# Optimization experiments

Measured on AMD Instinct MI355X. Metric: run time of the kernel, lower is better.

Reference implementation:

```python
import jax, jax.numpy as jnp
import numpy as np

D = 1024; H = 16; HD = 64; DEPTH = 8; INTERVAL = 4; CTX = 9; NUM_REG = 4
SOFTCAP = 50.0; EPS = 1e-6; ROPE_BASE = 10000.0; IN_DIM = 768; ADIM = 8; FREQ = 256; DH = 4096
B = 1; T = 16; LTOK = 256; S = LTOK + 2 + NUM_REG  # 262 tokens per frame


def setup_inputs() -> dict:
    key = jax.random.key(0)
    ks = jax.random.split(key, 24)
    s = 0.02
    n = jax.random.normal
    inp = {
        'noisy_latents': n(ks[0], (B, T, LTOK, IN_DIM), jnp.float32),
        'signal_levels': jax.random.uniform(ks[1], (B, T), jnp.float32),
        'actions': n(ks[2], (B, T, ADIM), jnp.float32),
        'input_proj_w': n(ks[3], (D, IN_DIM)) * s,
        'noise_w1': n(ks[4], (D, FREQ)) * s,
        'noise_b1': jnp.zeros((D,)),
        'noise_w2': n(ks[5], (D, D)) * s,
        'noise_b2': jnp.zeros((D,)),
        'base_action_embed': n(ks[6], (D,)) * s,
        'action_proj_w': n(ks[7], (D, ADIM)) * (s * 0.1),
        'action_proj_b': jnp.zeros((D,)),
        'register_tokens': n(ks[8], (NUM_REG, D)) * s,
        'ln1_w': jnp.ones((DEPTH, D)),
        's_wqkv': n(ks[9], (DEPTH, 3 * D, D)) * s,
        's_wo': n(ks[10], (DEPTH, D, D)) * s,
        's_qg': jnp.ones((DEPTH, HD)),
        's_kg': jnp.ones((DEPTH, HD)),
        'lnt_w': jnp.ones((DEPTH, D)),
        't_wqkv': n(ks[11], (DEPTH, 3 * D, D)) * s,
        't_wo': n(ks[12], (DEPTH, D, D)) * s,
        't_qg': jnp.ones((DEPTH, HD)),
        't_kg': jnp.ones((DEPTH, HD)),
        'ln2_w': jnp.ones((DEPTH, D)),
        'mlp_w12': n(ks[13], (DEPTH, 2 * DH, D)) * s,
        'mlp_w3': n(ks[14], (DEPTH, D, DH)) * s,
        'final_norm_w': jnp.ones((D,)),
        'out_w': n(ks[15], (IN_DIM, D)) * s,
        'out_b': jnp.zeros((IN_DIM,)),
    }
    return inp


def rms(x, w, eps=EPS):
    return x * jax.lax.rsqrt(jnp.mean(x * x, axis=-1, keepdims=True) + eps) * w


def rope_cache(seq_len):
    inv = ROPE_BASE ** (-jnp.arange(0, HD, 2, dtype=jnp.float32) / HD)  # [HD/2]
    f = jnp.arange(seq_len, dtype=jnp.float32)[:, None] * inv  # [S, HD/2]
    return jnp.cos(f), jnp.sin(f)


def apply_rope(x, cos, sin):
    # x: [..., S, HD]; cos/sin: [S, HD/2]
    x1, x2 = jnp.split(x, 2, axis=-1)
    return jnp.concatenate([x1 * cos - x2 * sin, x1 * sin + x2 * cos], axis=-1)


def attention(xn, wqkv, wo, qg, kg, cos, sin, mask):
    # xn: [B, G, S, D]; mask broadcastable to [..., S, S]
    lead = xn.shape[:-1]
    qkv = jnp.einsum('bgsd,ed->bgse', xn, wqkv)
    q, k, v = jnp.split(qkv, 3, axis=-1)
    def heads(z):
        return z.reshape(lead + (H, HD)).swapaxes(-2, -3)  # [B, G, H, S, HD]
    q, k, v = heads(q), heads(k), heads(v)
    q = rms(q, qg); k = rms(k, kg)  # qk-norm per head
    q = apply_rope(q, cos, sin); k = apply_rope(k, cos, sin)
    logits = jnp.einsum('bghqd,bghkd->bghqk', q, k) / np.sqrt(HD).astype(np.float32)
    logits = SOFTCAP * jnp.tanh(logits / SOFTCAP)  # attn logit softcapping
    logits = jnp.where(mask, logits, -1e30)
    p = jax.nn.softmax(logits, axis=-1)
    o = jnp.einsum('bghqk,bghkd->bghqd', p, v)
    o = o.swapaxes(-2, -3).reshape(lead + (H * HD,))
    return jnp.einsum('bgsd,ed->bgse', o, wo)


def timestep_embedding(t, dim=FREQ, max_period=10000.0):
    half = dim // 2
    freqs = jnp.exp(-np.log(max_period) * jnp.arange(half, dtype=jnp.float32) / half)
    args = t[:, None] * freqs
    return jnp.concatenate([jnp.cos(args), jnp.sin(args)], axis=-1)


def reference(noisy_latents, signal_levels, actions, input_proj_w, noise_w1, noise_b1,
              noise_w2, noise_b2, base_action_embed, action_proj_w, action_proj_b,
              register_tokens, ln1_w, s_wqkv, s_wo, s_qg, s_kg, lnt_w, t_wqkv, t_wo,
              t_qg, t_kg, ln2_w, mlp_w12, mlp_w3, final_norm_w, out_w, out_b):
    b, t, ltok, _ = noisy_latents.shape
    noisy_tokens = jnp.einsum('btld,ed->btle', noisy_latents, input_proj_w)  # [B,T,L,D]
    # timestep embedder (sinusoidal + MLP)
    emb = timestep_embedding(signal_levels.reshape(-1))
    sig = jax.nn.silu(emb @ noise_w1.T + noise_b1) @ noise_w2.T + noise_b2
    sig = sig.reshape(b, t, 1, D)
    act = base_action_embed + actions @ action_proj_w.T + action_proj_b  # [B,T,D]
    act = act[:, :, None, :]
    reg = jnp.broadcast_to(register_tokens, (b, t, NUM_REG, D))
    x = jnp.concatenate([sig, act, reg, noisy_tokens], axis=2)  # [B,T,S,D]
    s = x.shape[2]
    # spatial mask: full attention except frozen token (row 0) attends only to itself
    sm = jnp.ones((s, s), bool)
    sm = sm.at[0].set(False).at[0, 0].set(True)
    # temporal mask: causal with context window CTX
    ti = jnp.arange(t)
    tm = (ti[None, :] <= ti[:, None]) & (ti[None, :] >= ti[:, None] - CTX)
    s_cos, s_sin = rope_cache(s)
    t_cos, t_sin = rope_cache(t)
    for l in range(DEPTH):
        h = rms(x, ln1_w[l])
        x = x + attention(h, s_wqkv[l], s_wo[l], s_qg[l], s_kg[l], s_cos, s_sin, sm)
        if l % INTERVAL == 0:
            xt = x.swapaxes(1, 2)  # [B,S,T,D]
            h = rms(xt, lnt_w[l])
            xt = xt + attention(h, t_wqkv[l], t_wo[l], t_qg[l], t_kg[l], t_cos, t_sin, tm)
            x = xt.swapaxes(1, 2)
        h = rms(x, ln2_w[l])
        g = jnp.einsum('btsd,ed->btse', h, mlp_w12[l])
        g1, g2 = jnp.split(g, 2, axis=-1)
        x = x + jnp.einsum('btse,de->btsd', jax.nn.silu(g1) * g2, mlp_w3[l])
    latents = rms(x[..., NUM_REG + 2:, :], final_norm_w)
    return latents @ out_w.T + out_b  # [B,T,L,IN_DIM]
```

## Files before the change

### kernel.cpp

```cpp
#include <hip/hip_runtime.h>
#include <hip/hip_bf16.h>
#include <math.h>

#define T_ 16
#define S_ 262
#define D_ 1024
#define H_ 16
#define HD_ 64
#define DH_ 4096
#define NTOK (T_*S_)
#define LTOK_ 256
#define INDIM_ 768

typedef __attribute__((ext_vector_type(4))) float f32x4;
typedef __attribute__((ext_vector_type(8))) short s16x8;
typedef __attribute__((ext_vector_type(4))) short s16x4;

__device__ __forceinline__ short f2bf(float f) {
  union { float f; unsigned u; } v; v.f = f;
  unsigned r = v.u + 0x7fffu + ((v.u >> 16) & 1u);
  return (short)(r >> 16);
}
__device__ __forceinline__ float bf2f(short h) {
  union { unsigned u; float f; } v; v.u = ((unsigned)(unsigned short)h) << 16;
  return v.f;
}
__device__ __forceinline__ float softcap(float x) {
  float z = __expf(x * (2.0f / 50.0f));
  return 50.0f * (z - 1.0f) / (z + 1.0f);
}
__device__ __forceinline__ void gload16(const void* g, void* l) {
  __builtin_amdgcn_global_load_lds((const __attribute__((address_space(1))) void*)g,
                                   (__attribute__((address_space(3))) void*)l, 16, 0, 0);
}

template<int RESID, int BIAS, int OUT, int WB, int PERM, int PREP, int ROWMAP>
__global__ __launch_bounds__(256)
void gemm2(const short* __restrict__ A, const void* __restrict__ Wv,
           const float* __restrict__ bias, void* __restrict__ Cv,
           int M, int N, int K, int Ksub,
           const float* __restrict__ qg, const float* __restrict__ kg,
           const float* __restrict__ ctab, const float* __restrict__ stab)
{
  __shared__ __align__(16) short As[128*64];
  __shared__ __align__(16) short Bs[128*64];
  const int tid = threadIdx.x;
  const int m0 = blockIdx.y * 128, n0 = blockIdx.x * 128;
  const int lane = tid & 63, wid = tid >> 6;
  const int wr = (wid >> 1) * 64, wc = (wid & 1) * 64;
  const int lr = lane & 15, lk = (lane >> 4) * 8;
  const short* Wb = (const short*)Wv;
  const float* Wf = (const float*)Wv;

  const f32x4 fzero = {0.f, 0.f, 0.f, 0.f};
  f32x4 acc[4][4];
  #pragma unroll
  for (int i = 0; i < 4; ++i)
    #pragma unroll
    for (int j = 0; j < 4; ++j) acc[i][j] = fzero;

  const int kbeg = blockIdx.z * Ksub;
  for (int k0 = kbeg; k0 < kbeg + Ksub; k0 += 64) {
    #pragma unroll
    for (int i = 0; i < 4; ++i) {
      int row = wid*32 + i*8 + (lane >> 3);
      int gm = m0 + row; if (gm >= M) gm = M - 1;
      int gc = (((lane & 7) ^ (row & 7)) << 3);
      gload16(A + (size_t)gm*K + k0 + gc, &As[(wid*32 + i*8)*64]);
    }
    if (WB) {
      #pragma unroll
      for (int i = 0; i < 4; ++i) {
        int row = wid*32 + i*8 + (lane >> 3);
        int gc = (((lane & 7) ^ (row & 7)) << 3);
        gload16(Wb + (size_t)(n0 + row)*K + k0 + gc, &Bs[(wid*32 + i*8)*64]);
      }
    } else {
      #pragma unroll
      for (int i = 0; i < 4; ++i) {
        int slot = tid + 256*i;
        int row = slot >> 3, c8 = (slot & 7) << 3;
        int gr = n0 + row;
        if (PERM) { int c = gr >> 5, q = gr & 31; gr = (q < 16) ? c*16 + q : DH_ + c*16 + (q - 16); }
        const float* wp = Wf + (size_t)gr*K + k0 + c8;
        float4 w0 = *(const float4*)wp, w1 = *(const float4*)(wp + 4);
        s16x8 b;
        b[0]=f2bf(w0.x); b[1]=f2bf(w0.y); b[2]=f2bf(w0.z); b[3]=f2bf(w0.w);
        b[4]=f2bf(w1.x); b[5]=f2bf(w1.y); b[6]=f2bf(w1.z); b[7]=f2bf(w1.w);
        *(s16x8*)&Bs[row*64 + (c8 ^ ((row & 7) << 3))] = b;
      }
    }
    __syncthreads();
    #pragma unroll
    for (int kh = 0; kh < 2; ++kh) {
      const int col0 = kh*32 + lk;
      s16x8 af[4], bfr[4];
      #pragma unroll
      for (int mi = 0; mi < 4; ++mi) {
        int row = wr + mi*16 + lr;
        af[mi] = *(const s16x8*)&As[row*64 + (col0 ^ ((row & 7) << 3))];
      }
      #pragma unroll
      for (int ni = 0; ni < 4; ++ni) {
        int row = wc + ni*16 + lr;
        bfr[ni] = *(const s16x8*)&Bs[row*64 + (col0 ^ ((row & 7) << 3))];
      }
      #pragma unroll
      for (int mi = 0; mi < 4; ++mi)
        #pragma unroll
        for (int ni = 0; ni < 4; ++ni)
          acc[mi][ni] = __builtin_amdgcn_mfma_f32_16x16x32_bf16(af[mi], bfr[ni], acc[mi][ni], 0, 0, 0);
    }
    __syncthreads();
  }
  const int gg = (lane >> 4) * 4;
  if (OUT == 2) {
    #pragma unroll
    for (int mi = 0; mi < 4; ++mi)
      #pragma unroll
      for (int np = 0; np < 2; ++np) {
        const int ni = np*2;
        const int ocol = ((n0 + wc + ni*16) >> 5) * 16 + lr;
        #pragma unroll
        for (int r = 0; r < 4; ++r) {
          int row = m0 + wr + mi*16 + gg + r;
          if (row < M) {
            float g = acc[mi][ni][r], v = acc[mi][ni+1][r];
            float sl = g / (1.f + __expf(-g));
            ((short*)Cv)[(size_t)row * (N >> 1) + ocol] = f2bf(sl * v);
          }
        }
      }
  } else if (PREP) {
    const int colsec = n0 + wc;
    const bool isv = (colsec >= 2048);
    const float* gp = (colsec < 1024) ? qg : kg;
    float gv[4];
    if (!isv) {
      #pragma unroll
      for (int ni = 0; ni < 4; ++ni) gv[ni] = gp[ni*16 + lr];
    }
    #pragma unroll
    for (int mi = 0; mi < 4; ++mi) {
      #pragma unroll
      for (int r = 0; r < 4; ++r) {
        int row = m0 + wr + mi*16 + gg + r;
        int rowc = row < M ? row : M - 1;
        float vv[4];
        #pragma unroll
        for (int ni = 0; ni < 4; ++ni) vv[ni] = acc[mi][ni][r];
        if (!isv) {
          float ss = vv[0]*vv[0] + vv[1]*vv[1] + vv[2]*vv[2] + vv[3]*vv[3];
          ss += __shfl_xor(ss, 1);
          ss += __shfl_xor(ss, 2);
          ss += __shfl_xor(ss, 4);
          ss += __shfl_xor(ss, 8);
          float sc = rsqrtf(ss * (1.f/64.f) + 1e-6f);
          int pos = (PREP == 1) ? (rowc % S_) : (rowc / S_);
          float c0 = ctab[pos*32 + lr],      s0 = stab[pos*32 + lr];
          float c1 = ctab[pos*32 + 16 + lr], s1 = stab[pos*32 + 16 + lr];
          float a0 = vv[0]*sc*gv[0], a1 = vv[1]*sc*gv[1];
          float a2 = vv[2]*sc*gv[2], a3 = vv[3]*sc*gv[3];
          vv[0] = a0*c0 - a2*s0;
          vv[1] = a1*c1 - a3*s1;
          vv[2] = a0*s0 + a2*c0;
          vv[3] = a1*s1 + a3*c1;
        }
        if (row < M) {
          #pragma unroll
          for (int ni = 0; ni < 4; ++ni)
            ((short*)Cv)[(size_t)row * N + n0 + wc + ni*16 + lr] = f2bf(vv[ni]);
        }
      }
    }
  } else {
    #pragma unroll
    for (int mi = 0; mi < 4; ++mi)
      #pragma unroll
      for (int ni = 0; ni < 4; ++ni) {
        int col = n0 + wc + ni*16 + lr;
        #pragma unroll
        for (int r = 0; r < 4; ++r) {
          int row = m0 + wr + mi*16 + gg + r;
          if (row < M) {
            float v = acc[mi][ni][r];
            if (BIAS) v += bias[col];
            size_t orow = ROWMAP ? (size_t)((row >> 8) * S_ + 6 + (row & 255)) : (size_t)row;
            size_t idx = orow * N + col;
            if (RESID == 1)       ((float*)Cv)[idx] += v;
            else if (RESID == 2)  unsafeAtomicAdd(&((float*)Cv)[idx], v);
            else if (OUT == 1)    ((short*)Cv)[idx]  = f2bf(v);
            else                  ((float*)Cv)[idx]  = v;
          }
        }
      }
  }
}

template<int FINAL>
__global__ __launch_bounds__(256)
void rmsnorm_k(const float* __restrict__ x, const float* __restrict__ w, short* __restrict__ h)
{
  const int lane = threadIdx.x & 63;
  const int row = blockIdx.x*4 + (threadIdx.x >> 6);
  const int xrow = FINAL ? ((row >> 8) * S_ + 6 + (row & 255)) : row;
  const float* xp = x + (size_t)xrow*D_;
  float4 v[4];
  #pragma unroll
  for (int j = 0; j < 4; ++j) v[j] = *(const float4*)(xp + j*256 + lane*4);
  float ss = 0.f;
  #pragma unroll
  for (int j = 0; j < 4; ++j) ss += v[j].x*v[j].x + v[j].y*v[j].y + v[j].z*v[j].z + v[j].w*v[j].w;
  #pragma unroll
  for (int m = 1; m < 64; m <<= 1) ss += __shfl_xor(ss, m);
  const float sc = rsqrtf(ss * (1.f/1024.f) + 1e-6f);
  #pragma unroll
  for (int j = 0; j < 4; ++j) {
    float4 wv = *(const float4*)(w + j*256 + lane*4);
    s16x4 hv;
    hv[0] = f2bf(v[j].x*sc*wv.x); hv[1] = f2bf(v[j].y*sc*wv.y);
    hv[2] = f2bf(v[j].z*sc*wv.z); hv[3] = f2bf(v[j].w*sc*wv.w);
    *(s16x4*)(h + (size_t)row*D_ + j*256 + lane*4) = hv;
  }
}

__global__ void rope_tab_k(float* __restrict__ ct, float* __restrict__ st, int npos)
{
  int i = blockIdx.x*256 + threadIdx.x;
  if (i >= npos*32) return;
  int pos = i >> 5, fi = i & 31;
  float ang = (float)pos * expf((float)fi * (-9.210340371976184f/32.f));
  float s, c; sincosf(ang, &s, &c);
  ct[i] = c; st[i] = s;
}

__global__ __launch_bounds__(256)
void attn_spatial_k(const short* __restrict__ qkv, short* __restrict__ o)
{
  __shared__ __align__(16) short Vt[64][296];
  __shared__ __align__(16) short Pl[4][16][296];
  const int tid = threadIdx.x;
  const int b = blockIdx.x;
  const int t = b >> 4, h = b & 15;
// ... 105 lines not shown
  const int s = gw >> 4, h = gw & 15;
  const int tt = lane >> 2, dp = (lane & 3) * 16;
  const short* base = qkv + (size_t)(tt*S_ + s)*3072 + h*64 + dp;
  #pragma unroll
  for (int part = 0; part < 3; ++part) {
    const short* bp = base + part*1024;
    s16x8 v0 = *(const s16x8*)(bp);
    s16x8 v1 = *(const s16x8*)(bp + 8);
    float* dst = (part == 0) ? &Ql[wid][tt][dp] : (part == 1) ? &Kl[wid][tt][dp] : &Vl[wid][tt][dp];
    #pragma unroll
    for (int j = 0; j < 8; ++j) { dst[j] = bf2f(v0[j]); dst[8 + j] = bf2f(v1[j]); }
  }
  __syncthreads();
  const int qr = lane >> 2;
  float qv[64];
  #pragma unroll
  for (int j = 0; j < 64; ++j) qv[j] = Ql[wid][qr][j];
  float pvals[4];
  #pragma unroll
  for (int i = 0; i < 4; ++i) {
    int kt = (lane & 3) + i*4;
    float d = 0.f;
    #pragma unroll
    for (int j = 0; j < 64; ++j) d += qv[j] * Kl[wid][kt][j];
    d *= 0.125f;
    d = softcap(d);
    bool keep = (kt <= qr) && (kt + 9 >= qr);
    pvals[i] = keep ? d : -1e30f;
  }
  float mx = fmaxf(fmaxf(pvals[0], pvals[1]), fmaxf(pvals[2], pvals[3]));
  mx = fmaxf(mx, __shfl_xor(mx, 1));
  mx = fmaxf(mx, __shfl_xor(mx, 2));
  float sum = 0.f;
  #pragma unroll
  for (int i = 0; i < 4; ++i) { pvals[i] = __expf(pvals[i] - mx); sum += pvals[i]; }
  sum += __shfl_xor(sum, 1);
  sum += __shfl_xor(sum, 2);
  float is = 1.f / sum;
  #pragma unroll
  for (int i = 0; i < 4; ++i) Pl2[wid][qr][(lane & 3) + i*4] = pvals[i] * is;
  __syncthreads();
  float acc[16];
  #pragma unroll
  for (int j = 0; j < 16; ++j) acc[j] = 0.f;
  #pragma unroll
  for (int kt = 0; kt < 16; ++kt) {
    float pv = Pl2[wid][qr][kt];
    #pragma unroll
    for (int j = 0; j < 16; ++j) acc[j] += pv * Vl[wid][kt][dp + j];
  }
  short* op = o + (size_t)(qr*S_ + s)*D_ + h*64 + dp;
  #pragma unroll
  for (int j = 0; j < 16; ++j) op[j] = f2bf(acc[j]);
}

__global__ void cvt_f32_bf16_k(const float* __restrict__ in, short* __restrict__ out, int n4)
{
  int i = blockIdx.x*256 + threadIdx.x;
  if (i >= n4) return;
  float4 v = *(const float4*)(in + (size_t)i*4);
  s16x4 ov; ov[0]=f2bf(v.x); ov[1]=f2bf(v.y); ov[2]=f2bf(v.z); ov[3]=f2bf(v.w);
  *(s16x4*)(out + (size_t)i*4) = ov;
}

__global__ void cvt_w12_k(const float* __restrict__ in, short* __restrict__ out)
{
  int pb = blockIdx.x;
  int l = pb >> 13, pr = pb & 8191;
  int c = pr >> 5, q = pr & 31;
  int orig = (q < 16) ? c*16 + q : DH_ + c*16 + (q - 16);
  const float* ip = in + ((size_t)l*8192 + orig)*1024 + threadIdx.x*4;
  short* op = out + ((size_t)l*8192 + pr)*1024 + threadIdx.x*4;
  float4 v = *(const float4*)ip;
  s16x4 ov; ov[0]=f2bf(v.x); ov[1]=f2bf(v.y); ov[2]=f2bf(v.z); ov[3]=f2bf(v.w);
  *(s16x4*)op = ov;
}

__global__ void timestep_embed_k(const float* __restrict__ sig, float* __restrict__ emb)
{
  int tid = threadIdx.x;
  int n = tid >> 4;
  int j0 = (tid & 15) * 16;
  float tv = sig[n];
  for (int j = j0; j < j0 + 16; ++j) {
    int half = j & 127;
    float freq = expf(-9.210340371976184f * (float)half / 128.f);
    float a = tv * freq;
    emb[n*256 + j] = (j < 128) ? cosf(a) : sinf(a);
  }
}

__global__ void noise_mlp1_k(const float* __restrict__ emb, const float* __restrict__ w1,
                             const float* __restrict__ b1, float* __restrict__ hid)
{
  const int o = blockIdx.x*256 + threadIdx.x;
  const int n = o >> 10, e = o & 1023;
  const float4* er = (const float4*)(emb + n*256);
  const float4* wr = (const float4*)(w1 + (size_t)e*256);
  float s = b1[e];
  for (int k = 0; k < 64; ++k) { float4 a = er[k]; float4 b = wr[k]; s += a.x*b.x + a.y*b.y + a.z*b.z + a.w*b.w; }
  hid[o] = s / (1.f + __expf(-s));
}

__global__ void noise_mlp2_k(const float* __restrict__ hid, const float* __restrict__ w2,
                             const float* __restrict__ b2, float* __restrict__ sg)
{
// ... 43 lines not shown
  const float* nw1     = (const float*)d_in[4];
  const float* nb1     = (const float*)d_in[5];
  const float* nw2     = (const float*)d_in[6];
  const float* nb2     = (const float*)d_in[7];
  const float* base_ae = (const float*)d_in[8];
  const float* apw     = (const float*)d_in[9];
  const float* apb     = (const float*)d_in[10];
  const float* regtok  = (const float*)d_in[11];
  const float* ln1w    = (const float*)d_in[12];
  const float* s_wqkv  = (const float*)d_in[13];
  const float* s_wo    = (const float*)d_in[14];
  const float* s_qg    = (const float*)d_in[15];
  const float* s_kg    = (const float*)d_in[16];
  const float* lntw    = (const float*)d_in[17];
  const float* t_wqkv  = (const float*)d_in[18];
  const float* t_wo    = (const float*)d_in[19];
  const float* t_qg    = (const float*)d_in[20];
  const float* t_kg    = (const float*)d_in[21];
  const float* ln2w    = (const float*)d_in[22];
  const float* w12     = (const float*)d_in[23];
  const float* w3      = (const float*)d_in[24];
  const float* fnw     = (const float*)d_in[25];
  const float* outw    = (const float*)d_in[26];
  const float* outb    = (const float*)d_in[27];

  char* p = (char*)d_ws;
  auto take = [&](size_t n) { char* r = p; p += n; return r; };
  float* x   = (float*)take((size_t)NTOK*D_*4);
  short* hb  = (short*)take((size_t)NTOK*D_*2);
  short* qkv = (short*)take((size_t)NTOK*3072*2);
  short* ob  = (short*)take((size_t)NTOK*D_*2);
  short* mb  = qkv;
  short* nlb = (short*)take((size_t)4096*INDIM_*2);
  float* emb = (float*)take(16*256*4);
  float* hid = (float*)take(16*1024*4);
  float* sgb = (float*)take(16*1024*4);
  float* acr = (float*)take(16*1024*4);
  float* csS = (float*)take(S_*32*4);
  float* snS = (float*)take(S_*32*4);
  float* csT = (float*)take(16*32*4);
  float* snT = (float*)take(16*32*4);
  short* wqkv_s_bf = (short*)take((size_t)8*3*D_*D_*2);
  short* wo_s_bf   = (short*)take((size_t)8*D_*D_*2);
  short* wqkv_t_bf = (short*)take((size_t)2*3*D_*D_*2);
  short* wo_t_bf   = (short*)take((size_t)2*D_*D_*2);
  short* w12_bf    = (short*)take((size_t)8*2*DH_*D_*2);
  short* w3_bf     = (short*)take((size_t)8*D_*DH_*2);
  short* inp_bf    = (short*)take((size_t)D_*INDIM_*2);
  short* outw_bf   = (short*)take((size_t)INDIM_*D_*2);
  const size_t full_need = (size_t)(p - (char*)d_ws);
  const bool wb = ws_size >= full_need;

  if (wb) {
    cvt_f32_bf16_k<<<24576, 256, 0, stream>>>(s_wqkv, wqkv_s_bf, 8*3*D_*D_/4);
    cvt_f32_bf16_k<<<8192,  256, 0, stream>>>(s_wo,   wo_s_bf,   8*D_*D_/4);
    cvt_f32_bf16_k<<<3072,  256, 0, stream>>>(t_wqkv,                     wqkv_t_bf,                   3*D_*D_/4);
    cvt_f32_bf16_k<<<3072,  256, 0, stream>>>(t_wqkv + (size_t)4*3*D_*D_, wqkv_t_bf + (size_t)3*D_*D_, 3*D_*D_/4);
    cvt_f32_bf16_k<<<1024,  256, 0, stream>>>(t_wo,                       wo_t_bf,                     D_*D_/4);
    cvt_f32_bf16_k<<<1024,  256, 0, stream>>>(t_wo + (size_t)4*D_*D_,     wo_t_bf + (size_t)D_*D_,     D_*D_/4);
    cvt_w12_k<<<65536, 256, 0, stream>>>(w12, w12_bf);
    cvt_f32_bf16_k<<<32768, 256, 0, stream>>>(w3, w3_bf, 8*D_*DH_/4);
    cvt_f32_bf16_k<<<768,   256, 0, stream>>>(in_proj, inp_bf, D_*INDIM_/4);
    cvt_f32_bf16_k<<<768,   256, 0, stream>>>(outw, outw_bf, INDIM_*D_/4);
  }
  rope_tab_k<<<33, 256, 0, stream>>>(csS, snS, S_);
  rope_tab_k<<<2,  256, 0, stream>>>(csT, snT, 16);

  timestep_embed_k<<<1, 256, 0, stream>>>(sig_lv, emb);
  noise_mlp1_k<<<64, 256, 0, stream>>>(emb, nw1, nb1, hid);
  noise_mlp2_k<<<64, 256, 0, stream>>>(hid, nw2, nb2, sgb);
  act_embed_k<<<64, 256, 0, stream>>>(actions, base_ae, apw, apb, acr);
  cvt_f32_bf16_k<<<3072, 256, 0, stream>>>(noisy, nlb, 4096*INDIM_/4);
  if (wb) gemm2<0,0,0,1,0,0,1><<<dim3(8,32), 256, 0, stream>>>(nlb, inp_bf,  nullptr, x, 4096, D_, INDIM_, INDIM_, nullptr, nullptr, nullptr, nullptr);
  else    gemm2<0,0,0,0,0,0,1><<<dim3(8,32), 256, 0, stream>>>(nlb, in_proj, nullptr, x, 4096, D_, INDIM_, INDIM_, nullptr, nullptr, nullptr, nullptr);
  fill6_k<<<96, 256, 0, stream>>>(sgb, acr, regtok, x);

  for (int l = 0; l < 8; ++l) {
    rmsnorm_k<0><<<NTOK/4, 256, 0, stream>>>(x, ln1w + l*D_, hb);
    if (wb) gemm2<0,0,1,1,0,1,0><<<dim3(24,33), 256, 0, stream>>>(hb, wqkv_s_bf + (size_t)l*3*D_*D_, nullptr, qkv, NTOK, 3*D_, D_, D_, s_qg + l*HD_, s_kg + l*HD_, csS, snS);
    else    gemm2<0,0,1,0,0,1,0><<<dim3(24,33), 256, 0, stream>>>(hb, s_wqkv   + (size_t)l*3*D_*D_, nullptr, qkv, NTOK, 3*D_, D_, D_, s_qg + l*HD_, s_kg + l*HD_, csS, snS);
    attn_spatial_k<<<256, 256, 0, stream>>>(qkv, ob);
    if (wb) gemm2<1,0,0,1,0,0,0><<<dim3(8,33), 256, 0, stream>>>(ob, wo_s_bf + (size_t)l*D_*D_, nullptr, x, NTOK, D_, D_, D_, nullptr, nullptr, nullptr, nullptr);
    else    gemm2<1,0,0,0,0,0,0><<<dim3(8,33), 256, 0, stream>>>(ob, s_wo    + (size_t)l*D_*D_, nullptr, x, NTOK, D_, D_, D_, nullptr, nullptr, nullptr, nullptr);
    if (l % 4 == 0) {
      const int ls = l / 4;
      rmsnorm_k<0><<<NTOK/4, 256, 0, stream>>>(x, lntw + l*D_, hb);
      if (wb) gemm2<0,0,1,1,0,2,0><<<dim3(24,33), 256, 0, stream>>>(hb, wqkv_t_bf + (size_t)ls*3*D_*D_, nullptr, qkv, NTOK, 3*D_, D_, D_, t_qg + l*HD_, t_kg + l*HD_, csT, snT);
      else    gemm2<0,0,1,0,0,2,0><<<dim3(24,33), 256, 0, stream>>>(hb, t_wqkv    + (size_t)l*3*D_*D_,  nullptr, qkv, NTOK, 3*D_, D_, D_, t_qg + l*HD_, t_kg + l*HD_, csT, snT);
      attn_temporal_k<<<1048, 256, 0, stream>>>(qkv, ob);
      if (wb) gemm2<1,0,0,1,0,0,0><<<dim3(8,33), 256, 0, stream>>>(ob, wo_t_bf + (size_t)ls*D_*D_, nullptr, x, NTOK, D_, D_, D_, nullptr, nullptr, nullptr, nullptr);
      else    gemm2<1,0,0,0,0,0,0><<<dim3(8,33), 256, 0, stream>>>(ob, t_wo    + (size_t)l*D_*D_,  nullptr, x, NTOK, D_, D_, D_, nullptr, nullptr, nullptr, nullptr);
    }
    rmsnorm_k<0><<<NTOK/4, 256, 0, stream>>>(x, ln2w + l*D_, hb);
    if (wb) gemm2<0,0,2,1,0,0,0><<<dim3(64,33), 256, 0, stream>>>(hb, w12_bf + (size_t)l*2*DH_*D_, nullptr, mb, NTOK, 2*DH_, D_, D_, nullptr, nullptr, nullptr, nullptr);
    else    gemm2<0,0,2,0,1,0,0><<<dim3(64,33), 256, 0, stream>>>(hb, w12    + (size_t)l*2*DH_*D_, nullptr, mb, NTOK, 2*DH_, D_, D_, nullptr, nullptr, nullptr, nullptr);
    if (wb) gemm2<2,0,0,1,0,0,0><<<dim3(8,33,2), 256, 0, stream>>>(mb, w3_bf + (size_t)l*D_*DH_, nullptr, x, NTOK, D_, DH_, DH_/2, nullptr, nullptr, nullptr, nullptr);
    else    gemm2<2,0,0,0,0,0,0><<<dim3(8,33,2), 256, 0, stream>>>(mb, w3    + (size_t)l*D_*DH_, nullptr, x, NTOK, D_, DH_, DH_/2, nullptr, nullptr, nullptr, nullptr);
  }
  rmsnorm_k<1><<<1024, 256, 0, stream>>>(x, fnw, hb);
  if (wb) gemm2<0,1,0,1,0,0,0><<<dim3(6,32), 256, 0, stream>>>(hb, outw_bf, outb, (float*)d_out, 4096, INDIM_, D_, D_, nullptr, nullptr, nullptr, nullptr);
  else    gemm2<0,1,0,0,0,0,0><<<dim3(6,32), 256, 0, stream>>>(hb, outw,    outb, (float*)d_out, 4096, INDIM_, D_, D_, nullptr, nullptr, nullptr, nullptr);
}
```

Measured before the change: 3.386 ms.

## Add 64x64 GEMM tile variant for N=1024 GEMMs and drop split-K atomics

Adds a SMALL template mode giving 64x64 output tiles, and uses it for the narrow GEMMs (input projection, Wo projections, MLP down-projection, output head) so they launch more blocks. The down-projection no longer splits K with atomic adds and now accumulates over the full K=4096 in one block with a plain residual add. All weight conversions except w12 are batched into one multi-job conversion kernel. Smaller tiles lower data reuse per block and raise the number of loads per MFMA, in exchange for better occupancy and no atomic traffic.

```diff
diff --git a/kernel.cpp b/kernel.cpp
--- a/kernel.cpp
+++ b/kernel.cpp
@@ -34,50 +34,53 @@
                                    (__attribute__((address_space(3))) void*)l, 16, 0, 0);
 }
 
-template<int RESID, int BIAS, int OUT, int WB, int PERM, int PREP, int ROWMAP>
+template<int SMALL, int RESID, int BIAS, int OUT, int WB, int PERM, int PREP, int ROWMAP>
 __global__ __launch_bounds__(256)
 void gemm2(const short* __restrict__ A, const void* __restrict__ Wv,
            const float* __restrict__ bias, void* __restrict__ Cv,
-           int M, int N, int K, int Ksub,
+           int M, int N, int K,
            const float* __restrict__ qg, const float* __restrict__ kg,
            const float* __restrict__ ctab, const float* __restrict__ stab)
 {
-  __shared__ __align__(16) short As[128*64];
-  __shared__ __align__(16) short Bs[128*64];
+  constexpr int BM   = SMALL ? 64 : 128;
+  constexpr int MI   = SMALL ? 2 : 4;
+  constexpr int WR   = SMALL ? 32 : 64;
+  constexpr int NSTG = SMALL ? 2 : 4;
+  __shared__ __align__(16) short As[BM*64];
+  __shared__ __align__(16) short Bs[BM*64];
   const int tid = threadIdx.x;
-  const int m0 = blockIdx.y * 128, n0 = blockIdx.x * 128;
+  const int m0 = blockIdx.y * BM, n0 = blockIdx.x * BM;
   const int lane = tid & 63, wid = tid >> 6;
-  const int wr = (wid >> 1) * 64, wc = (wid & 1) * 64;
+  const int wr = (wid >> 1) * WR, wc = (wid & 1) * WR;
   const int lr = lane & 15, lk = (lane >> 4) * 8;
   const short* Wb = (const short*)Wv;
   const float* Wf = (const float*)Wv;
 
   const f32x4 fzero = {0.f, 0.f, 0.f, 0.f};
-  f32x4 acc[4][4];
-  #pragma unroll
-  for (int i = 0; i < 4; ++i)
-    #pragma unroll
-    for (int j = 0; j < 4; ++j) acc[i][j] = fzero;
-
-  const int kbeg = blockIdx.z * Ksub;
-  for (int k0 = kbeg; k0 < kbeg + Ksub; k0 += 64) {
-    #pragma unroll
-    for (int i = 0; i < 4; ++i) {
-      int row = wid*32 + i*8 + (lane >> 3);
+  f32x4 acc[MI][MI];
+  #pragma unroll
+  for (int i = 0; i < MI; ++i)
+    #pragma unroll
+    for (int j = 0; j < MI; ++j) acc[i][j] = fzero;
+
+  for (int k0 = 0; k0 < K; k0 += 64) {
+    #pragma unroll
+    for (int i = 0; i < NSTG; ++i) {
+      int row = wid*(NSTG*8) + i*8 + (lane >> 3);
       int gm = m0 + row; if (gm >= M) gm = M - 1;
       int gc = (((lane & 7) ^ (row & 7)) << 3);
-      gload16(A + (size_t)gm*K + k0 + gc, &As[(wid*32 + i*8)*64]);
+      gload16(A + (size_t)gm*K + k0 + gc, &As[(wid*(NSTG*8) + i*8)*64]);
     }
     if (WB) {
       #pragma unroll
-      for (int i = 0; i < 4; ++i) {
-        int row = wid*32 + i*8 + (lane >> 3);
+      for (int i = 0; i < NSTG; ++i) {
+        int row = wid*(NSTG*8) + i*8 + (lane >> 3);
         int gc = (((lane & 7) ^ (row & 7)) << 3);
-        gload16(Wb + (size_t)(n0 + row)*K + k0 + gc, &Bs[(wid*32 + i*8)*64]);
+        gload16(Wb + (size_t)(n0 + row)*K + k0 + gc, &Bs[(wid*(NSTG*8) + i*8)*64]);
       }
     } else {
       #pragma unroll
-      for (int i = 0; i < 4; ++i) {
+      for (int i = 0; i < NSTG; ++i) {
         int slot = tid + 256*i;
         int row = slot >> 3, c8 = (slot & 7) << 3;
         int gr = n0 + row;
@@ -94,31 +97,31 @@
     #pragma unroll
     for (int kh = 0; kh < 2; ++kh) {
       const int col0 = kh*32 + lk;
-      s16x8 af[4], bfr[4];
-      #pragma unroll
-      for (int mi = 0; mi < 4; ++mi) {
+      s16x8 af[MI], bfr[MI];
+      #pragma unroll
+      for (int mi = 0; mi < MI; ++mi) {
         int row = wr + mi*16 + lr;
         af[mi] = *(const s16x8*)&As[row*64 + (col0 ^ ((row & 7) << 3))];
       }
       #pragma unroll
-      for (int ni = 0; ni < 4; ++ni) {
+      for (int ni = 0; ni < MI; ++ni) {
         int row = wc + ni*16 + lr;
         bfr[ni] = *(const s16x8*)&Bs[row*64 + (col0 ^ ((row & 7) << 3))];
       }
       #pragma unroll
-      for (int mi = 0; mi < 4; ++mi)
+      for (int mi = 0; mi < MI; ++mi)
         #pragma unroll
-        for (int ni = 0; ni < 4; ++ni)
+        for (int ni = 0; ni < MI; ++ni)
           acc[mi][ni] = __builtin_amdgcn_mfma_f32_16x16x32_bf16(af[mi], bfr[ni], acc[mi][ni], 0, 0, 0);
     }
     __syncthreads();
   }
   const int gg = (lane >> 4) * 4;
-  if (OUT == 2) {
-    #pragma unroll
-    for (int mi = 0; mi < 4; ++mi)
-      #pragma unroll
-      for (int np = 0; np < 2; ++np) {
+  if constexpr (OUT == 2) {
+    #pragma unroll
+    for (int mi = 0; mi < MI; ++mi)
+      #pragma unroll
+      for (int np = 0; np < MI/2; ++np) {
         const int ni = np*2;
         const int ocol = ((n0 + wc + ni*16) >> 5) * 16 + lr;
         #pragma unroll
@@ -131,24 +134,24 @@
           }
         }
       }
-  } else if (PREP) {
+  } else if constexpr (PREP != 0) {
     const int colsec = n0 + wc;
     const bool isv = (colsec >= 2048);
     const float* gp = (colsec < 1024) ? qg : kg;
-    float gv[4];
+    float gv[MI];
     if (!isv) {
       #pragma unroll
-      for (int ni = 0; ni < 4; ++ni) gv[ni] = gp[ni*16 + lr];
-    }
-    #pragma unroll
-    for (int mi = 0; mi < 4; ++mi) {
+      for (int ni = 0; ni < MI; ++ni) gv[ni] = gp[ni*16 + lr];
+    }
+    #pragma unroll
+    for (int mi = 0; mi < MI; ++mi) {
       #pragma unroll
       for (int r = 0; r < 4; ++r) {
         int row = m0 + wr + mi*16 + gg + r;
         int rowc = row < M ? row : M - 1;
-        float vv[4];
+        float vv[MI];
         #pragma unroll
-        for (int ni = 0; ni < 4; ++ni) vv[ni] = acc[mi][ni][r];
+        for (int ni = 0; ni < MI; ++ni) vv[ni] = acc[mi][ni][r];
         if (!isv) {
           float ss = vv[0]*vv[0] + vv[1]*vv[1] + vv[2]*vv[2] + vv[3]*vv[3];
           ss += __shfl_xor(ss, 1);
@@ -168,16 +171,16 @@
         }
         if (row < M) {
           #pragma unroll
-          for (int ni = 0; ni < 4; ++ni)
+          for (int ni = 0; ni < MI; ++ni)
             ((short*)Cv)[(size_t)row * N + n0 + wc + ni*16 + lr] = f2bf(vv[ni]);
         }
       }
     }
   } else {
     #pragma unroll
-    for (int mi = 0; mi < 4; ++mi)
-      #pragma unroll
-      for (int ni = 0; ni < 4; ++ni) {
+    for (int mi = 0; mi < MI; ++mi)
+      #pragma unroll
+      for (int ni = 0; ni < MI; ++ni) {
         int col = n0 + wc + ni*16 + lr;
         #pragma unroll
         for (int r = 0; r < 4; ++r) {
@@ -188,7 +191,6 @@
             size_t orow = ROWMAP ? (size_t)((row >> 8) * S_ + 6 + (row & 255)) : (size_t)row;
             size_t idx = orow * N + col;
             if (RESID == 1)       ((float*)Cv)[idx] += v;
-            else if (RESID == 2)  unsafeAtomicAdd(&((float*)Cv)[idx], v);
             else if (OUT == 1)    ((short*)Cv)[idx]  = f2bf(v);
             else                  ((float*)Cv)[idx]  = v;
           }
@@ -400,6 +402,26 @@
   short* op = o + (size_t)(qr*S_ + s)*D_ + h*64 + dp;
   #pragma unroll
   for (int j = 0; j < 16; ++j) op[j] = f2bf(acc[j]);
+}
+
+struct CvtJobs {
+  const float* src[10];
+  short* dst[10];
+  int end[10];
+  int njobs;
+};
+
+__global__ void cvt_multi_k(CvtJobs jobs)
+{
+  int q = blockIdx.x*256 + threadIdx.x;
+  int j = 0;
+  while (j < jobs.njobs && q >= jobs.end[j]) ++j;
+  if (j >= jobs.njobs) return;
+  int base = (j == 0) ? 0 : jobs.end[j-1];
+  size_t idx = (size_t)(q - base);
+  float4 v = *(const float4*)(jobs.src[j] + idx*4);
+  s16x4 ov; ov[0]=f2bf(v.x); ov[1]=f2bf(v.y); ov[2]=f2bf(v.z); ov[3]=f2bf(v.w);
+  *(s16x4*)(jobs.dst[j] + idx*4) = ov;
 }
 
 __global__ void cvt_f32_bf16_k(const float* __restrict__ in, short* __restrict__ out, int n4)
@@ -549,16 +571,24 @@
   const bool wb = ws_size >= full_need;
 
   if (wb) {
-    cvt_f32_bf16_k<<<24576, 256, 0, stream>>>(s_wqkv, wqkv_s_bf, 8*3*D_*D_/4);
-    cvt_f32_bf16_k<<<8192,  256, 0, stream>>>(s_wo,   wo_s_bf,   8*D_*D_/4);
-    cvt_f32_bf16_k<<<3072,  256, 0, stream>>>(t_wqkv,                     wqkv_t_bf,                   3*D_*D_/4);
-    cvt_f32_bf16_k<<<3072,  256, 0, stream>>>(t_wqkv + (size_t)4*3*D_*D_, wqkv_t_bf + (size_t)3*D_*D_, 3*D_*D_/4);
-    cvt_f32_bf16_k<<<1024,  256, 0, stream>>>(t_wo,                       wo_t_bf,                     D_*D_/4);
-    cvt_f32_bf16_k<<<1024,  256, 0, stream>>>(t_wo + (size_t)4*D_*D_,     wo_t_bf + (size_t)D_*D_,     D_*D_/4);
+    CvtJobs jobs;
+    int acc_q = 0, nj = 0;
+    auto add = [&](const float* s, short* d, size_t elems) {
+      jobs.src[nj] = s; jobs.dst[nj] = d;
+      acc_q += (int)(elems / 4); jobs.end[nj] = acc_q; ++nj;
+    };
+    add(s_wqkv, wqkv_s_bf, (size_t)8*3*D_*D_);
+    add(s_wo,   wo_s_bf,   (size_t)8*D_*D_);
+    add(t_wqkv,                     wqkv_t_bf,                   (size_t)3*D_*D_);
+    add(t_wqkv + (size_t)4*3*D_*D_, wqkv_t_bf + (size_t)3*D_*D_, (size_t)3*D_*D_);
+    add(t_wo,                       wo_t_bf,                     (size_t)D_*D_);
+    add(t_wo + (size_t)4*D_*D_,     wo_t_bf + (size_t)D_*D_,     (size_t)D_*D_);
+    add(w3,   w3_bf,   (size_t)8*D_*DH_);
+    add(in_proj, inp_bf, (size_t)D_*INDIM_);
+    add(outw,    outw_bf,(size_t)INDIM_*D_);
+    jobs.njobs = nj;
+    cvt_multi_k<<<(acc_q + 255)/256, 256, 0, stream>>>(jobs);
     cvt_w12_k<<<65536, 256, 0, stream>>>(w12, w12_bf);
-    cvt_f32_bf16_k<<<32768, 256, 0, stream>>>(w3, w3_bf, 8*D_*DH_/4);
-    cvt_f32_bf16_k<<<768,   256, 0, stream>>>(in_proj, inp_bf, D_*INDIM_/4);
-    cvt_f32_bf16_k<<<768,   256, 0, stream>>>(outw, outw_bf, INDIM_*D_/4);
   }
   rope_tab_k<<<33, 256, 0, stream>>>(csS, snS, S_);
   rope_tab_k<<<2,  256, 0, stream>>>(csT, snT, 16);
@@ -568,33 +598,33 @@
   noise_mlp2_k<<<64, 256, 0, stream>>>(hid, nw2, nb2, sgb);
   act_embed_k<<<64, 256, 0, stream>>>(actions, base_ae, apw, apb, acr);
   cvt_f32_bf16_k<<<3072, 256, 0, stream>>>(noisy, nlb, 4096*INDIM_/4);
-  if (wb) gemm2<0,0,0,1,0,0,1><<<dim3(8,32), 256, 0, stream>>>(nlb, inp_bf,  nullptr, x, 4096, D_, INDIM_, INDIM_, nullptr, nullptr, nullptr, nullptr);
-  else    gemm2<0,0,0,0,0,0,1><<<dim3(8,32), 256, 0, stream>>>(nlb, in_proj, nullptr, x, 4096, D_, INDIM_, INDIM_, nullptr, nullptr, nullptr, nullptr);
+  if (wb) gemm2<1,0,0,0,1,0,0,1><<<dim3(16,64), 256, 0, stream>>>(nlb, inp_bf,  nullptr, x, 4096, D_, INDIM_, nullptr, nullptr, nullptr, nullptr);
+  else    gemm2<1,0,0,0,0,0,0,1><<<dim3(16,64), 256, 0, stream>>>(nlb, in_proj, nullptr, x, 4096, D_, INDIM_, nullptr, nullptr, nullptr, nullptr);
   fill6_k<<<96, 256, 0, stream>>>(sgb, acr, regtok, x);
 
   for (int l = 0; l < 8; ++l) {
     rmsnorm_k<0><<<NTOK/4, 256, 0, stream>>>(x, ln1w + l*D_, hb);
-    if (wb) gemm2<0,0,1,1,0,1,0><<<dim3(24,33), 256, 0, stream>>>(hb, wqkv_s_bf + (size_t)l*3*D_*D_, nullptr, qkv, NTOK, 3*D_, D_, D_, s_qg + l*HD_, s_kg + l*HD_, csS, snS);
-    else    gemm2<0,0,1,0,0,1,0><<<dim3(24,33), 256, 0, stream>>>(hb, s_wqkv   + (size_t)l*3*D_*D_, nullptr, qkv, NTOK, 3*D_, D_, D_, s_qg + l*HD_, s_kg + l*HD_, csS, snS);
+    if (wb) gemm2<0,0,0,1,1,0,1,0><<<dim3(24,33), 256, 0, stream>>>(hb, wqkv_s_bf + (size_t)l*3*D_*D_, nullptr, qkv, NTOK, 3*D_, D_, s_qg + l*HD_, s_kg + l*HD_, csS, snS);
+    else    gemm2<0,0,0,1,0,0,1,0><<<dim3(24,33), 256, 0, stream>>>(hb, s_wqkv   + (size_t)l*3*D_*D_, nullptr, qkv, NTOK, 3*D_, D_, s_qg + l*HD_, s_kg + l*HD_, csS, snS);
     attn_spatial_k<<<256, 256, 0, stream>>>(qkv, ob);
-    if (wb) gemm2<1,0,0,1,0,0,0><<<dim3(8,33), 256, 0, stream>>>(ob, wo_s_bf + (size_t)l*D_*D_, nullptr, x, NTOK, D_, D_, D_, nullptr, nullptr, nullptr, nullptr);
-    else    gemm2<1,0,0,0,0,0,0><<<dim3(8,33), 256, 0, stream>>>(ob, s_wo    + (size_t)l*D_*D_, nullptr, x, NTOK, D_, D_, D_, nullptr, nullptr, nullptr, nullptr);
+    if (wb) gemm2<1,1,0,0,1,0,0,0><<<dim3(16,66), 256, 0, stream>>>(ob, wo_s_bf + (size_t)l*D_*D_, nullptr, x, NTOK, D_, D_, nullptr, nullptr, nullptr, nullptr);
+    else    gemm2<1,1,0,0,0,0,0,0><<<dim3(16,66), 256, 0, stream>>>(ob, s_wo    + (size_t)l*D_*D_, nullptr, x, NTOK, D_, D_, nullptr, nullptr, nullptr, nullptr);
     if (l % 4 == 0) {
       const int ls = l / 4;
       rmsnorm_k<0><<<NTOK/4, 256, 0, stream>>>(x, lntw + l*D_, hb);
-      if (wb) gemm2<0,0,1,1,0,2,0><<<dim3(24,33), 256, 0, stream>>>(hb, wqkv_t_bf + (size_t)ls*3*D_*D_, nullptr, qkv, NTOK, 3*D_, D_, D_, t_qg + l*HD_, t_kg + l*HD_, csT, snT);
-      else    gemm2<0,0,1,0,0,2,0><<<dim3(24,33), 256, 0, stream>>>(hb, t_wqkv    + (size_t)l*3*D_*D_,  nullptr, qkv, NTOK, 3*D_, D_, D_, t_qg + l*HD_, t_kg + l*HD_, csT, snT);
+      if (wb) gemm2<0,0,0,1,1,0,2,0><<<dim3(24,33), 256, 0, stream>>>(hb, wqkv_t_bf + (size_t)ls*3*D_*D_, nullptr, qkv, NTOK, 3*D_, D_, t_qg + l*HD_, t_kg + l*HD_, csT, snT);
+      else    gemm2<0,0,0,1,0,0,2,0><<<dim3(24,33), 256, 0, stream>>>(hb, t_wqkv    + (size_t)l*3*D_*D_,  nullptr, qkv, NTOK, 3*D_, D_, t_qg + l*HD_, t_kg + l*HD_, csT, snT);
       attn_temporal_k<<<1048, 256, 0, stream>>>(qkv, ob);
-      if (wb) gemm2<1,0,0,1,0,0,0><<<dim3(8,33), 256, 0, stream>>>(ob, wo_t_bf + (size_t)ls*D_*D_, nullptr, x, NTOK, D_, D_, D_, nullptr, nullptr, nullptr, nullptr);
-      else    gemm2<1,0,0,0,0,0,0><<<dim3(8,33), 256, 0, stream>>>(ob, t_wo    + (size_t)l*D_*D_,  nullptr, x, NTOK, D_, D_, D_, nullptr, nullptr, nullptr, nullptr);
+      if (wb) gemm2<1,1,0,0,1,0,0,0><<<dim3(16,66), 256, 0, stream>>>(ob, wo_t_bf + (size_t)ls*D_*D_, nullptr, x, NTOK, D_, D_, nullptr, nullptr, nullptr, nullptr);
+      else    gemm2<1,1,0,0,0,0,0,0><<<dim3(16,66), 256, 0, stream>>>(ob, t_wo    + (size_t)l*D_*D_,  nullptr, x, NTOK, D_, D_, nullptr, nullptr, nullptr, nullptr);
     }
     rmsnorm_k<0><<<NTOK/4, 256, 0, stream>>>(x, ln2w + l*D_, hb);
-    if (wb) gemm2<0,0,2,1,0,0,0><<<dim3(64,33), 256, 0, stream>>>(hb, w12_bf + (size_t)l*2*DH_*D_, nullptr, mb, NTOK, 2*DH_, D_, D_, nullptr, nullptr, nullptr, nullptr);
-    else    gemm2<0,0,2,0,1,0,0><<<dim3(64,33), 256, 0, stream>>>(hb, w12    + (size_t)l*2*DH_*D_, nullptr, mb, NTOK, 2*DH_, D_, D_, nullptr, nullptr, nullptr, nullptr);
-    if (wb) gemm2<2,0,0,1,0,0,0><<<dim3(8,33,2), 256, 0, stream>>>(mb, w3_bf + (size_t)l*D_*DH_, nullptr, x, NTOK, D_, DH_, DH_/2, nullptr, nullptr, nullptr, nullptr);
-    else    gemm2<2,0,0,0,0,0,0><<<dim3(8,33,2), 256, 0, stream>>>(mb, w3    + (size_t)l*D_*DH_, nullptr, x, NTOK, D_, DH_, DH_/2, nullptr, nullptr, nullptr, nullptr);
+    if (wb) gemm2<0,0,0,2,1,0,0,0><<<dim3(64,33), 256, 0, stream>>>(hb, w12_bf + (size_t)l*2*DH_*D_, nullptr, mb, NTOK, 2*DH_, D_, nullptr, nullptr, nullptr, nullptr);
+    else    gemm2<0,0,0,2,0,1,0,0><<<dim3(64,33), 256, 0, stream>>>(hb, w12    + (size_t)l*2*DH_*D_, nullptr, mb, NTOK, 2*DH_, D_, nullptr, nullptr, nullptr, nullptr);
+    if (wb) gemm2<1,1,0,0,1,0,0,0><<<dim3(16,66), 256, 0, stream>>>(mb, w3_bf + (size_t)l*D_*DH_, nullptr, x, NTOK, D_, DH_, nullptr, nullptr, nullptr, nullptr);
+    else    gemm2<1,1,0,0,0,0,0,0><<<dim3(16,66), 256, 0, stream>>>(mb, w3    + (size_t)l*D_*DH_, nullptr, x, NTOK, D_, DH_, nullptr, nullptr, nullptr, nullptr);
   }
   rmsnorm_k<1><<<1024, 256, 0, stream>>>(x, fnw, hb);
-  if (wb) gemm2<0,1,0,1,0,0,0><<<dim3(6,32), 256, 0, stream>>>(hb, outw_bf, outb, (float*)d_out, 4096, INDIM_, D_, D_, nullptr, nullptr, nullptr, nullptr);
-  else    gemm2<0,1,0,0,0,0,0><<<dim3(6,32), 256, 0, stream>>>(hb, outw,    outb, (float*)d_out, 4096, INDIM_, D_, D_, nullptr, nullptr, nullptr, nullptr);
-}
+  if (wb) gemm2<1,0,1,0,1,0,0,0><<<dim3(12,64), 256, 0, stream>>>(hb, outw_bf, outb, (float*)d_out, 4096, INDIM_, D_, nullptr, nullptr, nullptr, nullptr);
+  else    gemm2<1,0,1,0,0,0,0,0><<<dim3(12,64), 256, 0, stream>>>(hb, outw,    outb, (float*)d_out, 4096, INDIM_, D_, nullptr, nullptr, nullptr, nullptr);
+}
```

Result: faster. 2.817 ms (-16.8%).

## Remap GEMM workgroups per XCD, drop split-K atomics, batch weight conversions

Applied to the files above, without the earlier changes.

Remaps the GEMM workgroup index so that consecutive tiles land on the same XCD, which should improve L2 reuse of shared A/B panels across the chiplets. The W3 down-projection no longer uses split-K with atomic adds. It runs the full K in one pass with a plain residual add, trading fewer workgroups for no atomics. Most fp32-to-bf16 weight and input conversions are merged into one multi-job launch to cut launch overhead.

```diff
diff --git a/kernel.cpp b/kernel.cpp
--- a/kernel.cpp
+++ b/kernel.cpp
@@ -38,14 +38,19 @@
 __global__ __launch_bounds__(256)
 void gemm2(const short* __restrict__ A, const void* __restrict__ Wv,
            const float* __restrict__ bias, void* __restrict__ Cv,
-           int M, int N, int K, int Ksub,
+           int M, int N, int K,
            const float* __restrict__ qg, const float* __restrict__ kg,
            const float* __restrict__ ctab, const float* __restrict__ stab)
 {
   __shared__ __align__(16) short As[128*64];
   __shared__ __align__(16) short Bs[128*64];
   const int tid = threadIdx.x;
-  const int m0 = blockIdx.y * 128, n0 = blockIdx.x * 128;
+  const int nwg = gridDim.x * gridDim.y;
+  const int orig = blockIdx.x + gridDim.x * blockIdx.y;
+  const int qq = nwg >> 3, rr = nwg & 7;
+  const int xcd = orig & 7, sidx = orig >> 3;
+  const int wg = (xcd < rr ? xcd*(qq+1) : rr*(qq+1) + (xcd-rr)*qq) + sidx;
+  const int m0 = (wg / gridDim.x) * 128, n0 = (wg % gridDim.x) * 128;
   const int lane = tid & 63, wid = tid >> 6;
   const int wr = (wid >> 1) * 64, wc = (wid & 1) * 64;
   const int lr = lane & 15, lk = (lane >> 4) * 8;
@@ -59,8 +64,7 @@
     #pragma unroll
     for (int j = 0; j < 4; ++j) acc[i][j] = fzero;
 
-  const int kbeg = blockIdx.z * Ksub;
-  for (int k0 = kbeg; k0 < kbeg + Ksub; k0 += 64) {
+  for (int k0 = 0; k0 < K; k0 += 64) {
     #pragma unroll
     for (int i = 0; i < 4; ++i) {
       int row = wid*32 + i*8 + (lane >> 3);
@@ -114,7 +118,7 @@
     __syncthreads();
   }
   const int gg = (lane >> 4) * 4;
-  if (OUT == 2) {
+  if constexpr (OUT == 2) {
     #pragma unroll
     for (int mi = 0; mi < 4; ++mi)
       #pragma unroll
@@ -131,7 +135,7 @@
           }
         }
       }
-  } else if (PREP) {
+  } else if constexpr (PREP != 0) {
     const int colsec = n0 + wc;
     const bool isv = (colsec >= 2048);
     const float* gp = (colsec < 1024) ? qg : kg;
@@ -188,7 +192,6 @@
             size_t orow = ROWMAP ? (size_t)((row >> 8) * S_ + 6 + (row & 255)) : (size_t)row;
             size_t idx = orow * N + col;
             if (RESID == 1)       ((float*)Cv)[idx] += v;
-            else if (RESID == 2)  unsafeAtomicAdd(&((float*)Cv)[idx], v);
             else if (OUT == 1)    ((short*)Cv)[idx]  = f2bf(v);
             else                  ((float*)Cv)[idx]  = v;
           }
@@ -400,6 +403,26 @@
   short* op = o + (size_t)(qr*S_ + s)*D_ + h*64 + dp;
   #pragma unroll
   for (int j = 0; j < 16; ++j) op[j] = f2bf(acc[j]);
+}
+
+struct CvtJobs {
+  const float* src[10];
+  short* dst[10];
+  int end[10];
+  int njobs;
+};
+
+__global__ void cvt_multi_k(CvtJobs jobs)
+{
+  int q = blockIdx.x*256 + threadIdx.x;
+  int j = 0;
+  while (j < jobs.njobs && q >= jobs.end[j]) ++j;
+  if (j >= jobs.njobs) return;
+  int base = (j == 0) ? 0 : jobs.end[j-1];
+  size_t idx = (size_t)(q - base);
+  float4 v = *(const float4*)(jobs.src[j] + idx*4);
+  s16x4 ov; ov[0]=f2bf(v.x); ov[1]=f2bf(v.y); ov[2]=f2bf(v.z); ov[3]=f2bf(v.w);
+  *(s16x4*)(jobs.dst[j] + idx*4) = ov;
 }
 
 __global__ void cvt_f32_bf16_k(const float* __restrict__ in, short* __restrict__ out, int n4)
@@ -549,16 +572,27 @@
   const bool wb = ws_size >= full_need;
 
   if (wb) {
-    cvt_f32_bf16_k<<<24576, 256, 0, stream>>>(s_wqkv, wqkv_s_bf, 8*3*D_*D_/4);
-    cvt_f32_bf16_k<<<8192,  256, 0, stream>>>(s_wo,   wo_s_bf,   8*D_*D_/4);
-    cvt_f32_bf16_k<<<3072,  256, 0, stream>>>(t_wqkv,                     wqkv_t_bf,                   3*D_*D_/4);
-    cvt_f32_bf16_k<<<3072,  256, 0, stream>>>(t_wqkv + (size_t)4*3*D_*D_, wqkv_t_bf + (size_t)3*D_*D_, 3*D_*D_/4);
-    cvt_f32_bf16_k<<<1024,  256, 0, stream>>>(t_wo,                       wo_t_bf,                     D_*D_/4);
-    cvt_f32_bf16_k<<<1024,  256, 0, stream>>>(t_wo + (size_t)4*D_*D_,     wo_t_bf + (size_t)D_*D_,     D_*D_/4);
+    CvtJobs jobs;
+    int acc_q = 0, nj = 0;
+    auto add = [&](const float* s, short* d, size_t elems) {
+      jobs.src[nj] = s; jobs.dst[nj] = d;
+      acc_q += (int)(elems / 4); jobs.end[nj] = acc_q; ++nj;
+    };
+    add(s_wqkv, wqkv_s_bf, (size_t)8*3*D_*D_);
+    add(s_wo,   wo_s_bf,   (size_t)8*D_*D_);
+    add(t_wqkv,                     wqkv_t_bf,                   (size_t)3*D_*D_);
+    add(t_wqkv + (size_t)4*3*D_*D_, wqkv_t_bf + (size_t)3*D_*D_, (size_t)3*D_*D_);
+    add(t_wo,                       wo_t_bf,                     (size_t)D_*D_);
+    add(t_wo + (size_t)4*D_*D_,     wo_t_bf + (size_t)D_*D_,     (size_t)D_*D_);
+    add(w3,   w3_bf,   (size_t)8*D_*DH_);
+    add(in_proj, inp_bf, (size_t)D_*INDIM_);
+    add(outw,    outw_bf,(size_t)INDIM_*D_);
+    add(noisy,   nlb,    (size_t)4096*INDIM_);
+    jobs.njobs = nj;
+    cvt_multi_k<<<(acc_q + 255)/256, 256, 0, stream>>>(jobs);
     cvt_w12_k<<<65536, 256, 0, stream>>>(w12, w12_bf);
-    cvt_f32_bf16_k<<<32768, 256, 0, stream>>>(w3, w3_bf, 8*D_*DH_/4);
-    cvt_f32_bf16_k<<<768,   256, 0, stream>>>(in_proj, inp_bf, D_*INDIM_/4);
-    cvt_f32_bf16_k<<<768,   256, 0, stream>>>(outw, outw_bf, INDIM_*D_/4);
+  } else {
+    cvt_f32_bf16_k<<<3072, 256, 0, stream>>>(noisy, nlb, 4096*INDIM_/4);
   }
   rope_tab_k<<<33, 256, 0, stream>>>(csS, snS, S_);
   rope_tab_k<<<2,  256, 0, stream>>>(csT, snT, 16);
@@ -567,34 +601,33 @@
   noise_mlp1_k<<<64, 256, 0, stream>>>(emb, nw1, nb1, hid);
   noise_mlp2_k<<<64, 256, 0, stream>>>(hid, nw2, nb2, sgb);
   act_embed_k<<<64, 256, 0, stream>>>(actions, base_ae, apw, apb, acr);
-  cvt_f32_bf16_k<<<3072, 256, 0, stream>>>(noisy, nlb, 4096*INDIM_/4);
-  if (wb) gemm2<0,0,0,1,0,0,1><<<dim3(8,32), 256, 0, stream>>>(nlb, inp_bf,  nullptr, x, 4096, D_, INDIM_, INDIM_, nullptr, nullptr, nullptr, nullptr);
-  else    gemm2<0,0,0,0,0,0,1><<<dim3(8,32), 256, 0, stream>>>(nlb, in_proj, nullptr, x, 4096, D_, INDIM_, INDIM_, nullptr, nullptr, nullptr, nullptr);
+  if (wb) gemm2<0,0,0,1,0,0,1><<<dim3(8,32), 256, 0, stream>>>(nlb, inp_bf,  nullptr, x, 4096, D_, INDIM_, nullptr, nullptr, nullptr, nullptr);
+  else    gemm2<0,0,0,0,0,0,1><<<dim3(8,32), 256, 0, stream>>>(nlb, in_proj, nullptr, x, 4096, D_, INDIM_, nullptr, nullptr, nullptr, nullptr);
   fill6_k<<<96, 256, 0, stream>>>(sgb, acr, regtok, x);
 
   for (int l = 0; l < 8; ++l) {
     rmsnorm_k<0><<<NTOK/4, 256, 0, stream>>>(x, ln1w + l*D_, hb);
-    if (wb) gemm2<0,0,1,1,0,1,0><<<dim3(24,33), 256, 0, stream>>>(hb, wqkv_s_bf + (size_t)l*3*D_*D_, nullptr, qkv, NTOK, 3*D_, D_, D_, s_qg + l*HD_, s_kg + l*HD_, csS, snS);
-    else    gemm2<0,0,1,0,0,1,0><<<dim3(24,33), 256, 0, stream>>>(hb, s_wqkv   + (size_t)l*3*D_*D_, nullptr, qkv, NTOK, 3*D_, D_, D_, s_qg + l*HD_, s_kg + l*HD_, csS, snS);
+    if (wb) gemm2<0,0,1,1,0,1,0><<<dim3(24,33), 256, 0, stream>>>(hb, wqkv_s_bf + (size_t)l*3*D_*D_, nullptr, qkv, NTOK, 3*D_, D_, s_qg + l*HD_, s_kg + l*HD_, csS, snS);
+    else    gemm2<0,0,1,0,0,1,0><<<dim3(24,33), 256, 0, stream>>>(hb, s_wqkv   + (size_t)l*3*D_*D_, nullptr, qkv, NTOK, 3*D_, D_, s_qg + l*HD_, s_kg + l*HD_, csS, snS);
     attn_spatial_k<<<256, 256, 0, stream>>>(qkv, ob);
-    if (wb) gemm2<1,0,0,1,0,0,0><<<dim3(8,33), 256, 0, stream>>>(ob, wo_s_bf + (size_t)l*D_*D_, nullptr, x, NTOK, D_, D_, D_, nullptr, nullptr, nullptr, nullptr);
-    else    gemm2<1,0,0,0,0,0,0><<<dim3(8,33), 256, 0, stream>>>(ob, s_wo    + (size_t)l*D_*D_, nullptr, x, NTOK, D_, D_, D_, nullptr, nullptr, nullptr, nullptr);
+    if (wb) gemm2<1,0,0,1,0,0,0><<<dim3(8,33), 256, 0, stream>>>(ob, wo_s_bf + (size_t)l*D_*D_, nullptr, x, NTOK, D_, D_, nullptr, nullptr, nullptr, nullptr);
+    else    gemm2<1,0,0,0,0,0,0><<<dim3(8,33), 256, 0, stream>>>(ob, s_wo    + (size_t)l*D_*D_, nullptr, x, NTOK, D_, D_, nullptr, nullptr, nullptr, nullptr);
     if (l % 4 == 0) {
       const int ls = l / 4;
       rmsnorm_k<0><<<NTOK/4, 256, 0, stream>>>(x, lntw + l*D_, hb);
-      if (wb) gemm2<0,0,1,1,0,2,0><<<dim3(24,33), 256, 0, stream>>>(hb, wqkv_t_bf + (size_t)ls*3*D_*D_, nullptr, qkv, NTOK, 3*D_, D_, D_, t_qg + l*HD_, t_kg + l*HD_, csT, snT);
-      else    gemm2<0,0,1,0,0,2,0><<<dim3(24,33), 256, 0, stream>>>(hb, t_wqkv    + (size_t)l*3*D_*D_,  nullptr, qkv, NTOK, 3*D_, D_, D_, t_qg + l*HD_, t_kg + l*HD_, csT, snT);
+      if (wb) gemm2<0,0,1,1,0,2,0><<<dim3(24,33), 256, 0, stream>>>(hb, wqkv_t_bf + (size_t)ls*3*D_*D_, nullptr, qkv, NTOK, 3*D_, D_, t_qg + l*HD_, t_kg + l*HD_, csT, snT);
+      else    gemm2<0,0,1,0,0,2,0><<<dim3(24,33), 256, 0, stream>>>(hb, t_wqkv    + (size_t)l*3*D_*D_,  nullptr, qkv, NTOK, 3*D_, D_, t_qg + l*HD_, t_kg + l*HD_, csT, snT);
       attn_temporal_k<<<1048, 256, 0, stream>>>(qkv, ob);
-      if (wb) gemm2<1,0,0,1,0,0,0><<<dim3(8,33), 256, 0, stream>>>(ob, wo_t_bf + (size_t)ls*D_*D_, nullptr, x, NTOK, D_, D_, D_, nullptr, nullptr, nullptr, nullptr);
-      else    gemm2<1,0,0,0,0,0,0><<<dim3(8,33), 256, 0, stream>>>(ob, t_wo    + (size_t)l*D_*D_,  nullptr, x, NTOK, D_, D_, D_, nullptr, nullptr, nullptr, nullptr);
+      if (wb) gemm2<1,0,0,1,0,0,0><<<dim3(8,33), 256, 0, stream>>>(ob, wo_t_bf + (size_t)ls*D_*D_, nullptr, x, NTOK, D_, D_, nullptr, nullptr, nullptr, nullptr);
+      else    gemm2<1,0,0,0,0,0,0><<<dim3(8,33), 256, 0, stream>>>(ob, t_wo    + (size_t)l*D_*D_,  nullptr, x, NTOK, D_, D_, nullptr, nullptr, nullptr, nullptr);
     }
     rmsnorm_k<0><<<NTOK/4, 256, 0, stream>>>(x, ln2w + l*D_, hb);
-    if (wb) gemm2<0,0,2,1,0,0,0><<<dim3(64,33), 256, 0, stream>>>(hb, w12_bf + (size_t)l*2*DH_*D_, nullptr, mb, NTOK, 2*DH_, D_, D_, nullptr, nullptr, nullptr, nullptr);
-    else    gemm2<0,0,2,0,1,0,0><<<dim3(64,33), 256, 0, stream>>>(hb, w12    + (size_t)l*2*DH_*D_, nullptr, mb, NTOK, 2*DH_, D_, D_, nullptr, nullptr, nullptr, nullptr);
-    if (wb) gemm2<2,0,0,1,0,0,0><<<dim3(8,33,2), 256, 0, stream>>>(mb, w3_bf + (size_t)l*D_*DH_, nullptr, x, NTOK, D_, DH_, DH_/2, nullptr, nullptr, nullptr, nullptr);
-    else    gemm2<2,0,0,0,0,0,0><<<dim3(8,33,2), 256, 0, stream>>>(mb, w3    + (size_t)l*D_*DH_, nullptr, x, NTOK, D_, DH_, DH_/2, nullptr, nullptr, nullptr, nullptr);
+    if (wb) gemm2<0,0,2,1,0,0,0><<<dim3(64,33), 256, 0, stream>>>(hb, w12_bf + (size_t)l*2*DH_*D_, nullptr, mb, NTOK, 2*DH_, D_, nullptr, nullptr, nullptr, nullptr);
+    else    gemm2<0,0,2,0,1,0,0><<<dim3(64,33), 256, 0, stream>>>(hb, w12    + (size_t)l*2*DH_*D_, nullptr, mb, NTOK, 2*DH_, D_, nullptr, nullptr, nullptr, nullptr);
+    if (wb) gemm2<1,0,0,1,0,0,0><<<dim3(8,33), 256, 0, stream>>>(mb, w3_bf + (size_t)l*D_*DH_, nullptr, x, NTOK, D_, DH_, nullptr, nullptr, nullptr, nullptr);
+    else    gemm2<1,0,0,0,0,0,0><<<dim3(8,33), 256, 0, stream>>>(mb, w3    + (size_t)l*D_*DH_, nullptr, x, NTOK, D_, DH_, nullptr, nullptr, nullptr, nullptr);
   }
   rmsnorm_k<1><<<1024, 256, 0, stream>>>(x, fnw, hb);
-  if (wb) gemm2<0,1,0,1,0,0,0><<<dim3(6,32), 256, 0, stream>>>(hb, outw_bf, outb, (float*)d_out, 4096, INDIM_, D_, D_, nullptr, nullptr, nullptr, nullptr);
-  else    gemm2<0,1,0,0,0,0,0><<<dim3(6,32), 256, 0, stream>>>(hb, outw,    outb, (float*)d_out, 4096, INDIM_, D_, D_, nullptr, nullptr, nullptr, nullptr);
-}
+  if (wb) gemm2<0,1,0,1,0,0,0><<<dim3(6,32), 256, 0, stream>>>(hb, outw_bf, outb, (float*)d_out, 4096, INDIM_, D_, nullptr, nullptr, nullptr, nullptr);
+  else    gemm2<0,1,0,0,0,0,0><<<dim3(6,32), 256, 0, stream>>>(hb, outw,    outb, (float*)d_out, 4096, INDIM_, D_, nullptr, nullptr, nullptr, nullptr);
+}
```

Result: no change. 3.428 ms (+1.2%).
